# Performance work log

Hardware: AMD Instinct MI355X
Metric: run time of the kernel (lower is better)

The kernel has to match this reference:

```python
import jax, jax.numpy as jnp
import numpy as np

N, E, Q = 50000, 800000, 2000000   # nodes, edges, quadruplets
F_IN, H, OUT, G = 128, 128, 1, 64  # in_channels, hidden, out_channels, graphs
NRBF = NCBF = NSBF = 6
L = 3  # num_layers


def _mlp2(h, Wa, ba, Wb, bb):
    # Linear -> ReLU -> Linear
    return jax.nn.relu(h @ Wa + ba) @ Wb + bb


def setup_inputs() -> dict:
    key = jax.random.key(0)
    ks = jax.random.split(key, 24)
    s = 0.05
    inp = {
        "x": jax.random.normal(ks[0], (N, F_IN), jnp.float32),
        "rbf": jax.random.normal(ks[1], (E, NRBF), jnp.float32),
        "cbf": jax.random.normal(ks[2], (Q, NCBF), jnp.float32),
        "sbf": jax.random.normal(ks[3], (Q, NSBF), jnp.float32),
        "edge_index": jax.random.randint(ks[4], (2, E), 0, N),
        "l_idx": jax.random.randint(ks[5], (Q,), 0, N),
        "k_idx": jax.random.randint(ks[6], (Q,), 0, E),
        "batch": jnp.sort(jax.random.randint(ks[7], (N,), 0, G)),
        # per-layer params (all layers share shapes since F_IN == H)
        "W_e1a": s * jax.random.normal(ks[8], (L, F_IN + NRBF + NCBF + NSBF, H)),
        "b_e1a": jnp.zeros((L, H)),
        "W_e1b": s * jax.random.normal(ks[9], (L, H, H)),
        "b_e1b": jnp.zeros((L, H)),
        "W_e2a": s * jax.random.normal(ks[10], (L, 2 * H, H)),
        "b_e2a": jnp.zeros((L, H)),
        "W_e2b": s * jax.random.normal(ks[11], (L, H, H)),
        "b_e2b": jnp.zeros((L, H)),
        "W_na": s * jax.random.normal(ks[12], (L, F_IN + H, H)),
        "b_na": jnp.zeros((L, H)),
        "W_nb": s * jax.random.normal(ks[13], (L, H, H)),
        "b_nb": jnp.zeros((L, H)),
        "W_oa": s * jax.random.normal(ks[14], (H, H)),
        "b_oa": jnp.zeros((H,)),
        "W_ob": s * jax.random.normal(ks[15], (H, OUT)),
        "b_ob": jnp.zeros((OUT,)),
    }
    return inp


def reference(x, rbf, cbf, sbf,
              W_e1a, b_e1a, W_e1b, b_e1b,
              W_e2a, b_e2a, W_e2b, b_e2b,
              W_na, b_na, W_nb, b_nb,
              W_oa, b_oa, W_ob, b_ob,
              edge_index, l_idx, k_idx, batch):
    src, dst = edge_index[0], edge_index[1]  # x_j = x[src], index = dst
    h = x
    for p in range(L):
        # quadruplet message: gather-concat-MLP  [Q, F+18] -> [Q, H]
        m_in = jnp.concatenate([h[l_idx], rbf[k_idx], cbf, sbf], axis=-1)
        em = _mlp2(m_in, W_e1a[p], b_e1a[p], W_e1b[p], b_e1b[p])
        # scatter-add quadruplet messages onto edges by k_idx -> [E, H]
        agg_e = jax.ops.segment_sum(em, k_idx, num_segments=E)
        # second stage: per-edge concat (note: aggregated indexed by dst, as in source)
        fin = jnp.concatenate([h[src], agg_e[dst]], axis=-1)
        msg = _mlp2(fin, W_e2a[p], b_e2a[p], W_e2b[p], b_e2b[p])
        # aggregate edge messages to target nodes -> [N, H]
        aggr = jax.ops.segment_sum(msg, dst, num_segments=N)
        h = _mlp2(jnp.concatenate([h, aggr], axis=-1), W_na[p], b_na[p], W_nb[p], b_nb[p])
    # global mean pool over graphs
    counts = jax.ops.segment_sum(jnp.ones((N, 1), h.dtype), batch, num_segments=G)
    pooled = jax.ops.segment_sum(h, batch, num_segments=G) / jnp.maximum(counts, 1.0)
    pooled = jax.nn.relu(pooled)
    return _mlp2(pooled, W_oa, b_oa, W_ob, b_ob)
```

## Files before the change

### kernel.cpp

```cpp
#include <hip/hip_runtime.h>

constexpr int Nn = 50000;
constexpr int Ee = 800000;
constexpr int Qq = 2000000;
constexpr int Gg = 64;
constexpr int Hh = 128;
constexpr int NB64 = (Nn + 63) / 64;
constexpr int NSCB = (Nn + 1023) / 1024;

typedef short bf16x8 __attribute__((ext_vector_type(8)));
typedef float f32x4  __attribute__((ext_vector_type(4)));

__device__ __forceinline__ unsigned short f2bf(float f) {
    unsigned u = __builtin_bit_cast(unsigned, f);
    u += 0x7FFFu + ((u >> 16) & 1u);
    return (unsigned short)(u >> 16);
}
__device__ __forceinline__ float bf2f(unsigned short s) {
    unsigned u = ((unsigned)s) << 16;
    return __builtin_bit_cast(float, u);
}

__global__ void k_hist2(const int* __restrict__ dst, const int* __restrict__ kidx,
                        int* __restrict__ hist_e, int* __restrict__ hist_q) {
    int i = blockIdx.x * blockDim.x + threadIdx.x;
    if (i < Ee) atomicAdd(&hist_e[dst[i]], 1);
    if (i < Qq) { int v = kidx[i]; if (v < Nn) atomicAdd(&hist_q[v], 1); }
}

__global__ __launch_bounds__(1024) void k_scanA2(const int* __restrict__ he,
                                                 const int* __restrict__ hq,
                                                 int* __restrict__ ce, int* __restrict__ cq,
                                                 int* __restrict__ bs) {
    __shared__ int s[1024];
    const int* h = blockIdx.y ? hq : he;
    int* c = blockIdx.y ? cq : ce;
    int* b = bs + blockIdx.y * 64;
    const int tid = threadIdx.x;
    int i = blockIdx.x * 1024 + tid;
    int v = (i < Nn) ? h[i] : 0;
    s[tid] = v;
    __syncthreads();
    for (int off = 1; off < 1024; off <<= 1) {
        int t = (tid >= off) ? s[tid - off] : 0;
        __syncthreads();
        s[tid] += t;
        __syncthreads();
    }
    if (i < Nn) c[i] = s[tid] - v;
    if (tid == 1023) b[blockIdx.x] = s[1023];
}
__global__ void k_scanB2(int* __restrict__ bs) {
    __shared__ int s[64];
    int* b = bs + blockIdx.x * 64;
    const int tid = threadIdx.x;
    int v = (tid < NSCB) ? b[tid] : 0;
    s[tid] = v;
    __syncthreads();
    for (int off = 1; off < 64; off <<= 1) {
        int t = (tid >= off) ? s[tid - off] : 0;
        __syncthreads();
        s[tid] += t;
        __syncthreads();
    }
    if (tid < NSCB) b[tid] = s[tid] - v;
}
__global__ __launch_bounds__(1024) void k_scanC2(int* __restrict__ ce, int* __restrict__ cq,
                                                 const int* __restrict__ bs) {
    int* c = blockIdx.y ? cq : ce;
    const int* b = bs + blockIdx.y * 64;
    int i = blockIdx.x * 1024 + threadIdx.x;
    if (i < Nn) c[i] += b[blockIdx.x];
}

__global__ void k_scatter_both(const int* __restrict__ dst, const int* __restrict__ src,
                               const int* __restrict__ kidx, const int* __restrict__ lidx,
                               const float* __restrict__ cbf, const float* __restrict__ sbf,
                               int* __restrict__ cur_e, int* __restrict__ cur_q,
                               int* __restrict__ srcs, unsigned short* __restrict__ qrec) {
    int i = blockIdx.x * blockDim.x + threadIdx.x;
    if (i < Ee) {
        int p = atomicAdd(&cur_e[dst[i]], 1);
        srcs[p] = src[i];
    }
    if (i < Qq) {
        int v = kidx[i];
        if (v < Nn) {
            int p = atomicAdd(&cur_q[v], 1);
            unsigned short rec[16];
            ((int*)rec)[0] = lidx[i];
#pragma unroll
            for (int k = 0; k < 6; ++k) rec[2 + k] = f2bf(cbf[(size_t)i * 6 + k]);
#pragma unroll
            for (int k = 0; k < 6; ++k) rec[8 + k] = f2bf(sbf[(size_t)i * 6 + k]);
            rec[14] = 0; rec[15] = 0;
            *(uint4*)&qrec[(size_t)p * 16]     = *(uint4*)&rec[0];
            *(uint4*)&qrec[(size_t)p * 16 + 8] = *(uint4*)&rec[8];
        }
    }
}

__global__ void k_wtall(const float* __restrict__ We1a0, const float* __restrict__ We1b0,
                        const float* __restrict__ We2a0, const float* __restrict__ We2b0,
                        const float* __restrict__ Wna0,  const float* __restrict__ Wnb0,
                        unsigned short* __restrict__ wbuf) {
    int idx = blockIdx.x * blockDim.x + threadIdx.x;
    if (idx >= 135168) return;
    const int p = blockIdx.y;
    const float* We1a = We1a0 + (size_t)p * 146 * 128;
    const float* We1b = We1b0 + (size_t)p * 128 * 128;
    const float* We2a = We2a0 + (size_t)p * 256 * 128;
    const float* We2b = We2b0 + (size_t)p * 128 * 128;
    const float* Wna  = Wna0  + (size_t)p * 256 * 128;
    const float* Wnb  = Wnb0  + (size_t)p * 128 * 128;
    unsigned short* base = wbuf + (size_t)p * 135168;
    const float* src; int K, Kp, loc;
    if (idx < 16384)       { src = We1a;             K = 128; Kp = 128; loc = idx; }
    else if (idx < 20480)  { src = We1a + 128 * 128; K = 6;   Kp = 32;  loc = idx - 16384; }
    else if (idx < 36864)  { src = We1b;             K = 128; Kp = 128; loc = idx - 20480; }
    else if (idx < 69632)  { src = We2a;             K = 256; Kp = 256; loc = idx - 36864; }
    else if (idx < 86016)  { src = We2b;             K = 128; Kp = 128; loc = idx - 69632; }
    else if (idx < 118784) { src = Wna;              K = 256; Kp = 256; loc = idx - 86016; }
    else                   { src = Wnb;              K = 128; Kp = 128; loc = idx - 118784; }
    int n = loc / Kp, k = loc - n * Kp;
    base[idx] = (k < K) ? f2bf(src[(size_t)k * 128 + n]) : (unsigned short)0;
}

__device__ __forceinline__ void zacc(f32x4 acc[4][2]) {
#pragma unroll
    for (int rt = 0; rt < 4; ++rt)
#pragma unroll
        for (int ct = 0; ct < 2; ++ct)
            acc[rt][ct] = (f32x4){0.f, 0.f, 0.f, 0.f};
}

template<int KK, int SA, int KP>
__device__ __forceinline__ void gemm64(const unsigned short* A,
                                       const unsigned short* __restrict__ Wt,
                                       int k_off, f32x4 acc[4][2]) {
    const int tid = threadIdx.x;
    const int lane = tid & 63;
    const int nb = (tid >> 6) * 32;
    const int rA = lane & 15;
    const int kg = lane >> 4;
#pragma unroll
    for (int ks = 0; ks < KK / 32; ++ks) {
        const int ka = ks * 32 + kg * 8;
        const int kb = k_off + ka;
        bf16x8 b0 = *(const bf16x8*)&Wt[(size_t)(nb + rA) * KP + kb];
        bf16x8 b1 = *(const bf16x8*)&Wt[(size_t)(nb + 16 + rA) * KP + kb];
#pragma unroll
        for (int rt = 0; rt < 4; ++rt) {
            bf16x8 a = *(const bf16x8*)&A[(rt * 16 + rA) * SA + ka];
            acc[rt][0] = __builtin_amdgcn_mfma_f32_16x16x32_bf16(a, b0, acc[rt][0], 0, 0, 0);
            acc[rt][1] = __builtin_amdgcn_mfma_f32_16x16x32_bf16(a, b1, acc[rt][1], 0, 0, 0);
        }
    }
}

__device__ __forceinline__ void store_acc(const f32x4 acc[4][2], unsigned short* out,
                                          int n0, int nmax) {
    const int tid = threadIdx.x;
    const int lane = tid & 63;
    const int nb = (tid >> 6) * 32;
    const int rA = lane & 15, kg = lane >> 4;
#pragma unroll
    for (int rt = 0; rt < 4; ++rt)
#pragma unroll
        for (int ct = 0; ct < 2; ++ct) {
            int col = nb + ct * 16 + rA;
#pragma unroll
            for (int i = 0; i < 4; ++i) {
                int n = n0 + rt * 16 + kg * 4 + i;
                if (n < nmax) out[(size_t)n * 128 + col] = f2bf(acc[rt][ct][i]);
            }
        }
}

__global__ __launch_bounds__(256) void k_pre0(
    const float* __restrict__ x, const float* __restrict__ rbf,
    const unsigned short* __restrict__ wbuf,
    unsigned short* __restrict__ hb,
    unsigned short* __restrict__ P1, unsigned short* __restrict__ Z1,
    unsigned short* __restrict__ P2all)
{
    __shared__ unsigned short TA[64 * 136];
    const int m0 = blockIdx.x * 64;
    const int tid = threadIdx.x;
    for (int i = tid; i < 64 * 32; i += 256) {
        int row = i >> 5, c = i & 31;
        int n = m0 + row;
        int nc = min(n, Nn - 1);
        float4 v = *(const float4*)&x[(size_t)nc * 128 + c * 4];
        ushort4 o;
        o.x = f2bf(v.x); o.y = f2bf(v.y); o.z = f2bf(v.z); o.w = f2bf(v.w);
        *(ushort4*)&TA[row * 136 + c * 4] = o;
        if (n < Nn) *(ushort4*)&hb[(size_t)n * 128 + c * 4] = o;
    }
    __syncthreads();
    f32x4 acc[4][2];
    zacc(acc);
    gemm64<128, 136, 128>(TA, wbuf, 0, acc);
    store_acc(acc, P1, m0, Nn);
    zacc(acc);
    gemm64<128, 136, 256>(TA, wbuf + 36864, 0, acc);
    store_acc(acc, Z1, m0, Nn);
    __syncthreads();
    for (int i = tid; i < 64 * 32; i += 256) {
        int row = i >> 5, c = i & 31;
        int nc = min(m0 + row, Nn - 1);
        float v = (c < 6) ? rbf[(size_t)nc * 6 + c] : 0.f;
        TA[row * 136 + c] = f2bf(v);
    }
    __syncthreads();
    for (int p = 0; p < 3; ++p) {
        zacc(acc);
        gemm64<32, 136, 32>(TA, wbuf + (size_t)p * 135168 + 16384, 0, acc);
        store_acc(acc, P2all + (size_t)p * Nn * 128, m0, Nn);
    }
}

__global__ __launch_bounds__(256) void k_quadagg(
    const unsigned short* __restrict__ P1, const unsigned short* __restrict__ P2,
    const unsigned short* __restrict__ qrec,
    const int* __restrict__ rowend, const int* __restrict__ rowcnt,
    const float* __restrict__ We1a_raw, const float* __restrict__ b_e1a,
    unsigned short* __restrict__ Rb)
{
    __shared__ float W34[12 * 128];
    __shared__ float bia[128];
    const int tid = threadIdx.x;
    for (int i = tid; i < 12 * 128; i += 256) W34[i] = We1a_raw[134 * 128 + i];
    if (tid < 128) bia[tid] = b_e1a[tid];
    __syncthreads();
    const int nd = tid >> 4;
    const int c0 = (tid & 15) * 8;
    const int n = blockIdx.x * 16 + nd;
    const int end = rowend[n];
    const int beg = end - rowcnt[n];
    float base[8];
    {
        uint4 p2v = *(const uint4*)&P2[(size_t)n * 128 + c0];
        const unsigned short* pp = (const unsigned short*)&p2v;
#pragma unroll
        for (int k = 0; k < 8; ++k) base[k] = bia[c0 + k] + bf2f(pp[k]);
    }
    float acc[8];
#pragma unroll
    for (int k = 0; k < 8; ++k) acc[k] = 0.f;
    for (int e = beg; e < end; ++e) {
        uint4 r0 = *(const uint4*)&qrec[(size_t)e * 16];
        uint4 r1 = *(const uint4*)&qrec[(size_t)e * 16 + 8];
        int l = ((const int*)&r0)[0];
        uint4 a = *(const uint4*)&P1[(size_t)l * 128 + c0];
        const unsigned short* q0 = (const unsigned short*)&r0;
        const unsigned short* q1 = (const unsigned short*)&r1;
        float qv[12] = {bf2f(q0[2]), bf2f(q0[3]), bf2f(q0[4]), bf2f(q0[5]),
                        bf2f(q0[6]), bf2f(q0[7]), bf2f(q1[0]), bf2f(q1[1]),
                        bf2f(q1[2]), bf2f(q1[3]), bf2f(q1[4]), bf2f(q1[5])};
        const unsigned short* ap = (const unsigned short*)&a;
        float t[8];
#pragma unroll
        for (int k = 0; k < 8; ++k) t[k] = base[k] + bf2f(ap[k]);
#pragma unroll
        for (int kk = 0; kk < 12; ++kk) {
            float q_ = qv[kk];
#pragma unroll
            for (int k = 0; k < 8; ++k)
                t[k] = fmaf(q_, W34[kk * 128 + c0 + k], t[k]);
        }
#pragma unroll
        for (int k = 0; k < 8; ++k) acc[k] += fmaxf(t[k], 0.f);
    }
    unsigned short ov[8];
#pragma unroll
    for (int k = 0; k < 8; ++k) ov[k] = f2bf(acc[k]);
    *(uint4*)&Rb[(size_t)n * 128 + c0] = *(uint4*)ov;
}

__global__ __launch_bounds__(256) void k_edgeagg(
    const unsigned short* __restrict__ Z1, const unsigned short* __restrict__ Z2,
    const int* __restrict__ srcs,
    const int* __restrict__ rowend, const int* __restrict__ rowcnt,
    const float* __restrict__ b_e2a,
    unsigned short* __restrict__ Rb)
{
    const int tid = threadIdx.x;
    const int nd = tid >> 4;
    const int c0 = (tid & 15) * 8;
    const int n = blockIdx.x * 16 + nd;
    const int end = rowend[n];
    const int beg = end - rowcnt[n];
    float z2b[8];
    {
        uint4 zv = *(const uint4*)&Z2[(size_t)n * 128 + c0];
        const unsigned short* zp = (const unsigned short*)&zv;
        float4 b0 = *(const float4*)&b_e2a[c0];
        float4 b1 = *(const float4*)&b_e2a[c0 + 4];
        z2b[0] = b0.x + bf2f(zp[0]); z2b[1] = b0.y + bf2f(zp[1]);
        z2b[2] = b0.z + bf2f(zp[2]); z2b[3] = b0.w + bf2f(zp[3]);
        z2b[4] = b1.x + bf2f(zp[4]); z2b[5] = b1.y + bf2f(zp[5]);
        z2b[6] = b1.z + bf2f(zp[6]); z2b[7] = b1.w + bf2f(zp[7]);
    }
    float acc[8];
#pragma unroll
    for (int k = 0; k < 8; ++k) acc[k] = 0.f;
    int e = beg;
    for (; e + 4 <= end; e += 4) {
        int s0 = srcs[e], s1 = srcs[e + 1], s2 = srcs[e + 2], s3 = srcs[e + 3];
        uint4 a0 = *(const uint4*)&Z1[(size_t)s0 * 128 + c0];
        uint4 a1 = *(const uint4*)&Z1[(size_t)s1 * 128 + c0];
        uint4 a2 = *(const uint4*)&Z1[(size_t)s2 * 128 + c0];
        uint4 a3 = *(const uint4*)&Z1[(size_t)s3 * 128 + c0];
        const unsigned short* p0 = (const unsigned short*)&a0;
        const unsigned short* p1 = (const unsigned short*)&a1;
        const unsigned short* p2 = (const unsigned short*)&a2;
        const unsigned short* p3 = (const unsigned short*)&a3;
#pragma unroll
        for (int k = 0; k < 8; ++k) acc[k] += fmaxf(z2b[k] + bf2f(p0[k]), 0.f);
#pragma unroll
        for (int k = 0; k < 8; ++k) acc[k] += fmaxf(z2b[k] + bf2f(p1[k]), 0.f);
#pragma unroll
        for (int k = 0; k < 8; ++k) acc[k] += fmaxf(z2b[k] + bf2f(p2[k]), 0.f);
#pragma unroll
        for (int k = 0; k < 8; ++k) acc[k] += fmaxf(z2b[k] + bf2f(p3[k]), 0.f);
    }
    for (; e + 2 <= end; e += 2) {
        int s0 = srcs[e], s1 = srcs[e + 1];
        uint4 a0 = *(const uint4*)&Z1[(size_t)s0 * 128 + c0];
        uint4 a1 = *(const uint4*)&Z1[(size_t)s1 * 128 + c0];
        const unsigned short* p0 = (const unsigned short*)&a0;
        const unsigned short* p1 = (const unsigned short*)&a1;
#pragma unroll
        for (int k = 0; k < 8; ++k) acc[k] += fmaxf(z2b[k] + bf2f(p0[k]), 0.f);
#pragma unroll
        for (int k = 0; k < 8; ++k) acc[k] += fmaxf(z2b[k] + bf2f(p1[k]), 0.f);
    }
    if (e < end) {
        int s0 = srcs[e];
        uint4 a0 = *(const uint4*)&Z1[(size_t)s0 * 128 + c0];
        const unsigned short* p0 = (const unsigned short*)&a0;
#pragma unroll
        for (int k = 0; k < 8; ++k) acc[k] += fmaxf(z2b[k] + bf2f(p0[k]), 0.f);
    }
    unsigned short ov[8];
#pragma unroll
    for (int k = 0; k < 8; ++k) ov[k] = f2bf(acc[k]);
    *(uint4*)&Rb[(size_t)n * 128 + c0] = *(uint4*)ov;
}

__global__ __launch_bounds__(256) void k_agg2z(
    const unsigned short* __restrict__ Rb, const int* __restrict__ cntq,
    const unsigned short* __restrict__ wb, const float* __restrict__ b_e1b,
    unsigned short* __restrict__ Z2)
{
    __shared__ unsigned short L[64 * 136];
    __shared__ int rc[64];
    const int m0 = blockIdx.x * 64;
    const int tid = threadIdx.x;
    const unsigned short* We1bt = wb + 20480;
    const unsigned short* We2at = wb + 36864;
    if (tid < 64) rc[tid] = (m0 + tid < Nn) ? cntq[m0 + tid] : 0;
    for (int i = tid; i < 64 * 16; i += 256) {
        int row = i >> 4, ch = i & 15;
        int n = min(m0 + row, Nn - 1);
        *(uint4*)&L[row * 136 + ch * 8] = *(const uint4*)&Rb[(size_t)n * 128 + ch * 8];
    }
    __syncthreads();
    f32x4 acc[4][2];
    zacc(acc);
    gemm64<128, 136, 128>(L, We1bt, 0, acc);
    __syncthreads();
    {
        const int lane = tid & 63;
        const int nb = (tid >> 6) * 32;
        const int rA = lane & 15, kg = lane >> 4;
#pragma unroll
        for (int rt = 0; rt < 4; ++rt)
#pragma unroll
            for (int ct = 0; ct < 2; ++ct) {
                int col = nb + ct * 16 + rA;
                float bias = b_e1b[col];
#pragma unroll
                for (int i = 0; i < 4; ++i) {
                    int row = rt * 16 + kg * 4 + i;
                    L[row * 136 + col] = f2bf(acc[rt][ct][i] + (float)rc[row] * bias);
                }
            }
    }
    __syncthreads();
    zacc(acc);
    gemm64<128, 136, 256>(L, We2at, 128, acc);
    store_acc(acc, Z2, m0, Nn);
}

template<int LAST>
__global__ __launch_bounds__(256) void k_nodeNew(
    const unsigned short* __restrict__ Rb, const int* __restrict__ deg,
    const unsigned short* __restrict__ wb,
    const float* __restrict__ b_e2b, const float* __restrict__ b_na,
    const float* __restrict__ b_nb,
    unsigned short* __restrict__ hb,
    const unsigned short* __restrict__ wbn,
    unsigned short* __restrict__ P1n, unsigned short* __restrict__ Z1n)
{
    __shared__ unsigned short L[64 * 136];
    __shared__ int rc[64];
    const int m0 = blockIdx.x * 64;
    const int tid = threadIdx.x;
    const unsigned short* We2bt = wb + 69632;
    const unsigned short* Wnat  = wb + 86016;
    const unsigned short* Wnbt  = wb + 118784;
    const int lane = tid & 63;
    const int nb = (tid >> 6) * 32;
    const int rA = lane & 15, kg = lane >> 4;
    if (tid < 64) rc[tid] = (m0 + tid < Nn) ? deg[m0 + tid] : 0;
    for (int i = tid; i < 64 * 16; i += 256) {
        int row = i >> 4, ch = i & 15;
        int n = min(m0 + row, Nn - 1);
        *(uint4*)&L[row * 136 + ch * 8] = *(const uint4*)&Rb[(size_t)n * 128 + ch * 8];
    }
    __syncthreads();
    f32x4 acc[4][2];
    zacc(acc);
    gemm64<128, 136, 128>(L, We2bt, 0, acc);
    __syncthreads();
#pragma unroll
    for (int rt = 0; rt < 4; ++rt)
#pragma unroll
        for (int ct = 0; ct < 2; ++ct) {
            int col = nb + ct * 16 + rA;
            float bias = b_e2b[col];
#pragma unroll
            for (int i = 0; i < 4; ++i) {
                int row = rt * 16 + kg * 4 + i;
                L[row * 136 + col] = f2bf(acc[rt][ct][i] + (float)rc[row] * bias);
            }
        }
    __syncthreads();
    f32x4 acc2[4][2];
    zacc(acc2);
    gemm64<128, 136, 256>(L, Wnat, 128, acc2);
    __syncthreads();
    for (int i = tid; i < 64 * 16; i += 256) {
        int row = i >> 4, ch = i & 15;
        int n = min(m0 + row, Nn - 1);
        *(uint4*)&L[row * 136 + ch * 8] = *(const uint4*)&hb[(size_t)n * 128 + ch * 8];
    }
    __syncthreads();
    gemm64<128, 136, 256>(L, Wnat, 0, acc2);
    __syncthreads();
#pragma unroll
    for (int rt = 0; rt < 4; ++rt)
#pragma unroll
        for (int ct = 0; ct < 2; ++ct) {
            int col = nb + ct * 16 + rA;
            float bias = b_na[col];
#pragma unroll
            for (int i = 0; i < 4; ++i) {
                int row = rt * 16 + kg * 4 + i;
                L[row * 136 + col] = f2bf(fmaxf(acc2[rt][ct][i] + bias, 0.f));
            }
        }
    __syncthreads();
    zacc(acc);
    gemm64<128, 136, 128>(L, Wnbt, 0, acc);
    __syncthreads();
#pragma unroll
    for (int rt = 0; rt < 4; ++rt)
#pragma unroll
        for (int ct = 0; ct < 2; ++ct) {
            int col = nb + ct * 16 + rA;
            float bias = b_nb[col];
#pragma unroll
            for (int i = 0; i < 4; ++i) {
                int row = rt * 16 + kg * 4 + i;
                int n = m0 + row;
                unsigned short hv = f2bf(acc[rt][ct][i] + bias);
                if (n < Nn) hb[(size_t)n * 128 + col] = hv;
                if (!LAST) L[row * 136 + col] = hv;
            }
        }
    if (!LAST) {
        __syncthreads();
        zacc(acc);
        gemm64<128, 136, 128>(L, wbn, 0, acc);
        store_acc(acc, P1n, m0, Nn);
        zacc(acc);
        gemm64<128, 136, 256>(L, wbn + 36864, 0, acc);
        store_acc(acc, Z1n, m0, Nn);
    }
}

__global__ __launch_bounds__(256) void k_pool(const unsigned short* __restrict__ hb,
                                              const int* __restrict__ batch,
                                              float* __restrict__ pooled,
                                              float* __restrict__ cntg) {
    __shared__ int bseg[200];
    constexpr int CH = 196;
    const int start = blockIdx.x * CH;
    const int end = min(start + CH, Nn);
    if (start >= end) return;
    const int tid = threadIdx.x;
    for (int i = tid; i < end - start; i += 256) bseg[i] = batch[start + i];
    __syncthreads();
    const int j = tid & 127;
    const int rh = tid >> 7;
    float acc = 0.f, cacc = 0.f;
    int cur = -1;
    for (int n = start + rh; n < end; n += 2) {
        int g = bseg[n - start];
        if (g != cur) {
            if (cur >= 0) {
                atomicAdd(&pooled[cur * Hh + j], acc);
                if (j == 0) atomicAdd(&cntg[cur], cacc);
            }
            cur = g; acc = 0.f; cacc = 0.f;
        }
        acc += bf2f(hb[(size_t)n * Hh + j]);
        cacc += 1.f;
    }
    if (cur >= 0) {
        atomicAdd(&pooled[cur * Hh + j], acc);
        if (j == 0) atomicAdd(&cntg[cur], cacc);
    }
}

__global__ __launch_bounds__(128) void k_final(
    const float* __restrict__ pooled, const float* __restrict__ cntg,
    const float* __restrict__ Woa, const float* __restrict__ boa,
    const float* __restrict__ Wob, const float* __restrict__ bob,
    float* __restrict__ out)
{
    __shared__ float p[128];
    __shared__ float t[128];
    __shared__ float red[128];
    const int g = blockIdx.x;
    const int j = threadIdx.x;
    float c = fmaxf(cntg[g], 1.f);
    p[j] = fmaxf(pooled[g * Hh + j] / c, 0.f);
    __syncthreads();
    float acc = boa[j];
    for (int d = 0; d < Hh; ++d) acc = fmaf(p[d], Woa[d * Hh + j], acc);
    t[j] = fmaxf(acc, 0.f);
    __syncthreads();
    red[j] = t[j] * Wob[j];
    __syncthreads();
    for (int s = 64; s > 0; s >>= 1) {
        if (j < s) red[j] += red[j + s];
        __syncthreads();
    }
    if (j == 0) out[g] = red[0] + bob[0];
}

extern "C" void kernel_launch(void* const* d_in, const int* in_sizes, int n_in,
                              void* d_out, int out_size, void* d_ws, size_t ws_size,
                              hipStream_t stream) {
    const float* x     = (const float*)d_in[0];
    const float* rbf   = (const float*)d_in[1];
    const float* cbf   = (const float*)d_in[2];
    const float* sbf   = (const float*)d_in[3];
    const int*   eidx  = (const int*)d_in[4];
    const int*   l_idx = (const int*)d_in[5];
    const int*   k_idx = (const int*)d_in[6];
    const int*   batch = (const int*)d_in[7];
    const float* W_e1a = (const float*)d_in[8];
    const float* b_e1a = (const float*)d_in[9];
    const float* W_e1b = (const float*)d_in[10];
    const float* b_e1b = (const float*)d_in[11];
    const float* W_e2a = (const float*)d_in[12];
    const float* b_e2a = (const float*)d_in[13];
    const float* W_e2b = (const float*)d_in[14];
    const float* b_e2b = (const float*)d_in[15];
    const float* W_na  = (const float*)d_in[16];
    const float* b_na  = (const float*)d_in[17];
    const float* W_nb  = (const float*)d_in[18];
    const float* b_nb  = (const float*)d_in[19];
    const float* W_oa  = (const float*)d_in[20];
    const float* b_oa  = (const float*)d_in[21];
    const float* W_ob  = (const float*)d_in[22];
    const float* b_ob  = (const float*)d_in[23];

    const int* src = eidx;
    const int* dst = eidx + Ee;

    const size_t NHb = (size_t)Nn * Hh * sizeof(unsigned short);
    char* w = (char*)d_ws;
    unsigned short* hb   = (unsigned short*)w; w += NHb;
    unsigned short* P1a  = (unsigned short*)w; w += NHb;
    unsigned short* P1b  = (unsigned short*)w; w += NHb;
    unsigned short* Z1a  = (unsigned short*)w; w += NHb;
    unsigned short* Z1b  = (unsigned short*)w; w += NHb;
    unsigned short* Z2   = (unsigned short*)w; w += NHb;
    unsigned short* Rb   = (unsigned short*)w; w += NHb;
    unsigned short* P2all = (unsigned short*)w; w += 3 * NHb;
    float* pooled = (float*)w; w += (size_t)Gg * Hh * sizeof(float);
    float* cntg   = (float*)w; w += (size_t)Gg * sizeof(float);
    unsigned short* qrec = (unsigned short*)w; w += (size_t)Qq * 16 * sizeof(unsigned short);
    int*   srcs_e = (int*)w;   w += (size_t)Ee * sizeof(int);
    int*   hist_e = (int*)w;   w += (size_t)Nn * sizeof(int);
    int*   hist_q = (int*)w;   w += (size_t)Nn * sizeof(int);
    int*   cur_e  = (int*)w;   w += (size_t)Nn * sizeof(int);
    int*   cur_q  = (int*)w;   w += (size_t)Nn * sizeof(int);
    int*   bsum   = (int*)w;   w += 128 * sizeof(int);
    unsigned short* wbuf = (unsigned short*)w;

    const size_t LSTRIDE = 135168;

    hipMemsetAsync(hist_e, 0, 2 * (size_t)Nn * sizeof(int), stream);
    k_hist2<<<(Qq + 255) / 256, 256, 0, stream>>>(dst, k_idx, hist_e, hist_q);
    {
        dim3 g(NSCB, 2);
        k_scanA2<<<g, 1024, 0, stream>>>(hist_e, hist_q, cur_e, cur_q, bsum);
        k_scanB2<<<2, 64, 0, stream>>>(bsum);
        k_scanC2<<<g, 1024, 0, stream>>>(cur_e, cur_q, bsum);
    }
    k_scatter_both<<<(Qq + 255) / 256, 256, 0, stream>>>(dst, src, k_idx, l_idx,
        cbf, sbf, cur_e, cur_q, srcs_e, qrec);

    {
        dim3 g((135168 + 255) / 256, 3);
        k_wtall<<<g, 256, 0, stream>>>(W_e1a, W_e1b, W_e2a, W_e2b, W_na, W_nb, wbuf);
    }
    k_pre0<<<NB64, 256, 0, stream>>>(x, rbf, wbuf, hb, P1a, Z1a, P2all);

    unsigned short* P1s[2] = { P1a, P1b };
    unsigned short* Z1s[2] = { Z1a, Z1b };
    for (int p = 0; p < 3; ++p) {
        const unsigned short* wb = wbuf + p * LSTRIDE;
        const unsigned short* wbn = wbuf + ((p + 1) % 3) * LSTRIDE;
        int c = p & 1;
        k_quadagg<<<Nn / 16, 256, 0, stream>>>(P1s[c],
            P2all + (size_t)p * Nn * 128, qrec, cur_q, hist_q,
            W_e1a + (size_t)p * 146 * 128, b_e1a + (size_t)p * 128, Rb);
        k_agg2z<<<NB64, 256, 0, stream>>>(Rb, hist_q, wb, b_e1b + (size_t)p * 128, Z2);
        k_edgeagg<<<Nn / 16, 256, 0, stream>>>(Z1s[c], Z2, srcs_e, cur_e, hist_e,
            b_e2a + (size_t)p * 128, Rb);
        if (p < 2)
            k_nodeNew<0><<<NB64, 256, 0, stream>>>(Rb, hist_e, wb,
                b_e2b + (size_t)p * 128, b_na + (size_t)p * 128, b_nb + (size_t)p * 128,
                hb, wbn, P1s[c ^ 1], Z1s[c ^ 1]);
        else
            k_nodeNew<1><<<NB64, 256, 0, stream>>>(Rb, hist_e, wb,
                b_e2b + (size_t)p * 128, b_na + (size_t)p * 128, b_nb + (size_t)p * 128,
                hb, wbn, P1s[c ^ 1], Z1s[c ^ 1]);
    }
    hipMemsetAsync(pooled, 0, (size_t)(Gg * Hh + Gg) * sizeof(float), stream);
    k_pool<<<(Nn + 195) / 196, 256, 0, stream>>>(hb, batch, pooled, cntg);
    k_final<<<Gg, 128, 0, stream>>>(pooled, cntg, W_oa, b_oa, W_ob, b_ob, (float*)d_out);
}
```

Baseline: 531.1 us.

## Bucket edge CSR scatter by groups of 16 nodes with LDS-atomic finalize

Replaces the per-destination global atomic scatter of edge sources with a two-level scheme. Edges are first scattered into 16-node buckets, with the source id and the local node index packed into one word. A finalize kernel then places each edge into its final CSR slot using shared-memory atomics. This is meant to make the writes more coherent, at the cost of an extra kernel pass, a staging buffer, and packing src into 16 bits, which assumes N fits in 65536.

Result: slower. 566.7 us (+6.7%).

```diff
diff --git a/kernel.cpp b/kernel.cpp
--- a/kernel.cpp
+++ b/kernel.cpp
@@ -7,6 +7,7 @@
 constexpr int Hh = 128;
 constexpr int NB64 = (Nn + 63) / 64;
 constexpr int NSCB = (Nn + 1023) / 1024;
+constexpr int NBUK = Nn / 16;
 
 typedef short bf16x8 __attribute__((ext_vector_type(8)));
 typedef float f32x4  __attribute__((ext_vector_type(4)));
@@ -73,15 +74,22 @@
     if (i < Nn) c[i] += b[blockIdx.x];
 }
 
+__global__ void k_bukinit(const int* __restrict__ cur_e, int* __restrict__ ebcur) {
+    int b = blockIdx.x * blockDim.x + threadIdx.x;
+    if (b < NBUK) ebcur[b] = cur_e[b * 16];
+}
+
 __global__ void k_scatter_both(const int* __restrict__ dst, const int* __restrict__ src,
                                const int* __restrict__ kidx, const int* __restrict__ lidx,
                                const float* __restrict__ cbf, const float* __restrict__ sbf,
-                               int* __restrict__ cur_e, int* __restrict__ cur_q,
-                               int* __restrict__ srcs, unsigned short* __restrict__ qrec) {
+                               int* __restrict__ ebcur, int* __restrict__ cur_q,
+                               unsigned* __restrict__ estage,
+                               unsigned short* __restrict__ qrec) {
     int i = blockIdx.x * blockDim.x + threadIdx.x;
     if (i < Ee) {
-        int p = atomicAdd(&cur_e[dst[i]], 1);
-        srcs[p] = src[i];
+        int d = dst[i];
+        int p = atomicAdd(&ebcur[d >> 4], 1);
+        estage[p] = (unsigned)src[i] | ((unsigned)(d & 15) << 16);
     }
     if (i < Qq) {
         int v = kidx[i];
@@ -97,6 +105,25 @@
             *(uint4*)&qrec[(size_t)p * 16]     = *(uint4*)&rec[0];
             *(uint4*)&qrec[(size_t)p * 16 + 8] = *(uint4*)&rec[8];
         }
+    }
+}
+
+__global__ __launch_bounds__(256) void k_finalize(
+    const unsigned* __restrict__ estage, const int* __restrict__ cur_e,
+    const int* __restrict__ hist_e, int* __restrict__ srcs) {
+    __shared__ int lcur[16];
+    const int b = blockIdx.x;
+    const int tid = threadIdx.x;
+    const int n0 = b * 16;
+    if (tid < 16) lcur[tid] = cur_e[n0 + tid];
+    __syncthreads();
+    const int beg = cur_e[n0];
+    const int end = cur_e[n0 + 15] + hist_e[n0 + 15];
+    for (int i = beg + tid; i < end; i += 256) {
+        unsigned pk = estage[i];
+        int nd = (pk >> 16) & 15;
+        int p = atomicAdd(&lcur[nd], 1);
+        srcs[p] = (int)(pk & 0xFFFFu);
     }
 }
 
@@ -281,7 +308,7 @@
 __global__ __launch_bounds__(256) void k_edgeagg(
     const unsigned short* __restrict__ Z1, const unsigned short* __restrict__ Z2,
     const int* __restrict__ srcs,
-    const int* __restrict__ rowend, const int* __restrict__ rowcnt,
+    const int* __restrict__ rowbeg, const int* __restrict__ rowcnt,
     const float* __restrict__ b_e2a,
     unsigned short* __restrict__ Rb)
 {
@@ -289,8 +316,8 @@
     const int nd = tid >> 4;
     const int c0 = (tid & 15) * 8;
     const int n = blockIdx.x * 16 + nd;
-    const int end = rowend[n];
-    const int beg = end - rowcnt[n];
+    const int beg = rowbeg[n];
+    const int end = beg + rowcnt[n];
     float z2b[8];
     {
         uint4 zv = *(const uint4*)&Z2[(size_t)n * 128 + c0];
@@ -598,10 +625,12 @@
     float* cntg   = (float*)w; w += (size_t)Gg * sizeof(float);
     unsigned short* qrec = (unsigned short*)w; w += (size_t)Qq * 16 * sizeof(unsigned short);
     int*   srcs_e = (int*)w;   w += (size_t)Ee * sizeof(int);
+    unsigned* estage = (unsigned*)w; w += (size_t)Ee * sizeof(unsigned);
     int*   hist_e = (int*)w;   w += (size_t)Nn * sizeof(int);
     int*   hist_q = (int*)w;   w += (size_t)Nn * sizeof(int);
     int*   cur_e  = (int*)w;   w += (size_t)Nn * sizeof(int);
     int*   cur_q  = (int*)w;   w += (size_t)Nn * sizeof(int);
+    int*   ebcur  = (int*)w;   w += (size_t)NBUK * sizeof(int);
     int*   bsum   = (int*)w;   w += 128 * sizeof(int);
     unsigned short* wbuf = (unsigned short*)w;
 
@@ -615,8 +644,10 @@
         k_scanB2<<<2, 64, 0, stream>>>(bsum);
         k_scanC2<<<g, 1024, 0, stream>>>(cur_e, cur_q, bsum);
     }
+    k_bukinit<<<(NBUK + 255) / 256, 256, 0, stream>>>(cur_e, ebcur);
     k_scatter_both<<<(Qq + 255) / 256, 256, 0, stream>>>(dst, src, k_idx, l_idx,
-        cbf, sbf, cur_e, cur_q, srcs_e, qrec);
+        cbf, sbf, ebcur, cur_q, estage, qrec);
+    k_finalize<<<NBUK, 256, 0, stream>>>(estage, cur_e, hist_e, srcs_e);
 
     {
         dim3 g((135168 + 255) / 256, 3);
```
